# Kernel optimization log

Measured on AMD Instinct MI355X. Metric: run time of the kernel, lower is better.

The kernel has to match this reference:

```python
import math
import jax, jax.numpy as jnp
import numpy as np

D_MODEL = 256
N_HEADS = 8
D_K = D_MODEL // N_HEADS
BS = 2
SEQ = 2048
NEG = -1e32


def _linear(x, W, b):
    return x @ W + b


def _layernorm(x, g, b):
    m = jnp.mean(x, axis=-1, keepdims=True)
    v = jnp.mean((x - m) ** 2, axis=-1, keepdims=True)
    return (x - m) / jnp.sqrt(v + 1e-5) * g + b


def _attention(q, k, v, mask, gammas):
    # q,k,v: [b,h,s,dk]; mask: [1,1,s,s] bool; gammas: [h,1,1]
    d_k = q.shape[-1]
    scores = jnp.einsum('bhqd,bhkd->bhqk', q, k) / math.sqrt(d_k)
    S = scores.shape[-1]
    # distance-decay bias (computed under stop_gradient, as torch.no_grad + detach)
    sm = jax.lax.stop_gradient(jax.nn.softmax(jnp.where(mask, scores, NEG), axis=-1))
    distcum = jnp.cumsum(sm, axis=-1)
    disttot = jnp.sum(sm, axis=-1, keepdims=True)
    idx = jnp.arange(S, dtype=scores.dtype)
    pos = jnp.abs(idx[None, :] - idx[:, None])[None, None]  # |i-j|
    dist = jax.lax.stop_gradient(
        jnp.sqrt(jnp.clip((disttot - distcum) * pos, 0.0, None)))
    gamma = -jax.nn.softplus(gammas)[None]  # [1,h,1,1]
    eff = jnp.clip(jnp.exp(dist * gamma), 1e-5, 1e5)
    scores = jnp.where(mask, scores * eff, NEG)
    scores = jnp.where(mask, jax.nn.softmax(scores, axis=-1), 0.0)
    return jnp.einsum('bhqk,bhkd->bhqd', scores, v)


def _mha(qx, kx, vx, Wq, bq, Wk, bk, Wv, bv, Wo, bo, gammas, mask):
    bs = qx.shape[0]
    def split(x, W, b):
        return _linear(x, W, b).reshape(bs, -1, N_HEADS, D_K).transpose(0, 2, 1, 3)
    q = split(qx, Wq, bq)
    k = split(kx, Wk, bk)
    v = split(vx, Wv, bv)
    o = _attention(q, k, v, mask, gammas)
    o = o.transpose(0, 2, 1, 3).reshape(bs, -1, D_MODEL)
    return _linear(o, Wo, bo)


def _layer(query, key, values, Wq, bq, Wk, bk, Wv, bv, Wo, bo, gammas, ln_g, ln_b, peek_cur):
    S = query.shape[1]
    mask = jnp.tril(jnp.ones((S, S), dtype=bool), 0 if peek_cur else -1)[None, None]
    out = _mha(query, key, values, Wq, bq, Wk, bk, Wv, bv, Wo, bo, gammas, mask)
    return _layernorm(query + out, ln_g, ln_b)


def _forward(q_emb, qa_emb,
             b1_Wq, b1_bq, b1_Wv, b1_bv, b1_Wo, b1_bo, b1_gam, b1_lng, b1_lnb,
             b2_Wq, b2_bq, b2_Wv, b2_bv, b2_Wo, b2_bo, b2_gam, b2_lng, b2_lnb,
             b3_Wq, b3_bq, b3_Wk, b3_bk, b3_Wv, b3_bv, b3_Wo, b3_bo, b3_gam, b3_lng, b3_lnb,
             know_params, lk_W, lk_b, lv_W, lv_b):
    # blocks 1 & 2: kq_same -> k projection shares q projection weights
    hq = _layer(q_emb, q_emb, q_emb,
                b1_Wq, b1_bq, b1_Wq, b1_bq, b1_Wv, b1_bv, b1_Wo, b1_bo,
                b1_gam, b1_lng, b1_lnb, peek_cur=True)
    ha = _layer(qa_emb, qa_emb, qa_emb,
                b2_Wq, b2_bq, b2_Wq, b2_bq, b2_Wv, b2_bv, b2_Wo, b2_bo,
                b2_gam, b2_lng, b2_lnb, peek_cur=True)
    query = jnp.broadcast_to(know_params, hq.shape)
    h = _layer(query, hq, ha,
               b3_Wq, b3_bq, b3_Wk, b3_bk, b3_Wv, b3_bv, b3_Wo, b3_bo,
               b3_gam, b3_lng, b3_lnb, peek_cur=False)
    bs, S, d = hq.shape
    key = jax.nn.sigmoid(_linear(
        jnp.broadcast_to(know_params, (bs, S, d)).reshape(bs, S, N_HEADS, D_K),
        lk_W, lk_b)).reshape(bs * S, N_HEADS, d)
    value = jax.nn.sigmoid(_linear(
        h.reshape(bs, S, N_HEADS, D_K), lv_W, lv_b)).reshape(bs * S, N_HEADS, d)
    beta = jnp.einsum('nhd,nd->nh', key, q_emb.reshape(bs * S, d))
    alpha = jax.nn.softmax(beta, axis=-1)
    h = jnp.einsum('nh,nhd->nd', alpha, value).reshape(bs, S, d)
    return h


def setup_inputs() -> dict:
    keys = iter(jax.random.split(jax.random.key(0), 64))
    def nrm(shape, scale=0.02):
        return jax.random.normal(next(keys), shape, dtype=jnp.float32) * scale
    def uni(shape):
        return jax.random.uniform(next(keys), shape, dtype=jnp.float32, minval=-1.0, maxval=1.0)
    d = D_MODEL
    inp = {
        'q_emb': nrm((BS, SEQ, d), 1.0),
        'qa_emb': nrm((BS, SEQ, d), 1.0),
    }
    for blk in ('b1', 'b2'):
        inp[blk + '_Wq'] = nrm((d, d)); inp[blk + '_bq'] = jnp.zeros((d,), jnp.float32)
        inp[blk + '_Wv'] = nrm((d, d)); inp[blk + '_bv'] = jnp.zeros((d,), jnp.float32)
        inp[blk + '_Wo'] = nrm((d, d)); inp[blk + '_bo'] = jnp.zeros((d,), jnp.float32)
        inp[blk + '_gam'] = uni((N_HEADS, 1, 1))
        inp[blk + '_lng'] = jnp.ones((d,), jnp.float32)
        inp[blk + '_lnb'] = jnp.zeros((d,), jnp.float32)
    inp['b3_Wq'] = nrm((d, d)); inp['b3_bq'] = jnp.zeros((d,), jnp.float32)
    inp['b3_Wk'] = nrm((d, d)); inp['b3_bk'] = jnp.zeros((d,), jnp.float32)
    inp['b3_Wv'] = nrm((d, d)); inp['b3_bv'] = jnp.zeros((d,), jnp.float32)
    inp['b3_Wo'] = nrm((d, d)); inp['b3_bo'] = jnp.zeros((d,), jnp.float32)
    inp['b3_gam'] = uni((N_HEADS, 1, 1))
    inp['b3_lng'] = jnp.ones((d,), jnp.float32)
    inp['b3_lnb'] = jnp.zeros((d,), jnp.float32)
    inp['know_params'] = uni((1, 1, d))
    inp['lk_W'] = nrm((D_K, d)); inp['lk_b'] = jnp.zeros((d,), jnp.float32)
    inp['lv_W'] = nrm((D_K, d)); inp['lv_b'] = jnp.zeros((d,), jnp.float32)
    return inp


def reference(q_emb, qa_emb,
              b1_Wq, b1_bq, b1_Wv, b1_bv, b1_Wo, b1_bo, b1_gam, b1_lng, b1_lnb,
              b2_Wq, b2_bq, b2_Wv, b2_bv, b2_Wo, b2_bo, b2_gam, b2_lng, b2_lnb,
              b3_Wq, b3_bq, b3_Wk, b3_bk, b3_Wv, b3_bv, b3_Wo, b3_bo, b3_gam, b3_lng, b3_lnb,
              know_params, lk_W, lk_b, lv_W, lv_b):
    return _forward(q_emb, qa_emb,
                    b1_Wq, b1_bq, b1_Wv, b1_bv, b1_Wo, b1_bo, b1_gam, b1_lng, b1_lnb,
                    b2_Wq, b2_bq, b2_Wv, b2_bv, b2_Wo, b2_bo, b2_gam, b2_lng, b2_lnb,
                    b3_Wq, b3_bq, b3_Wk, b3_bk, b3_Wv, b3_bv, b3_Wo, b3_bo, b3_gam, b3_lng, b3_lnb,
                    know_params, lk_W, lk_b, lv_W, lv_b)
```

## Files before the change

kernel.cpp:

```cpp
#include <hip/hip_runtime.h>
#include <hip/hip_bf16.h>

#define DM 256
#define NH 8
#define DK 32
#define BSZ 2
#define SEQ 2048
#define ROWS (BSZ*SEQ)
#define RT 16
#define SRB 2312

static __device__ __forceinline__ int sw8(int j) { return j + ((j >> 6) << 3); }

typedef __attribute__((ext_vector_type(8))) short short8;
typedef __attribute__((ext_vector_type(4))) float f32x4;

static __device__ __forceinline__ unsigned short f2bf(float f) {
    unsigned u = __float_as_uint(f);
    return (unsigned short)((u + 0x7FFFu + ((u >> 16) & 1u)) >> 16);
}
static __device__ __forceinline__ float bf2f(unsigned short h) {
    return __uint_as_float(((unsigned)h) << 16);
}

static __device__ __forceinline__ unsigned cvtpk(float lo, float hi) {
    unsigned r;
    asm("v_cvt_pk_bf16_f32 %0, %1, %2" : "=v"(r) : "v"(lo), "v"(hi));
    return r;
}

static __device__ __forceinline__ float ex2(float x) { return __builtin_amdgcn_exp2f(x); }
static __device__ __forceinline__ float sqt(float x) { return __builtin_amdgcn_sqrtf(x); }
static __device__ __forceinline__ float rcp(float x) { return __builtin_amdgcn_rcpf(x); }

template<int CTRL, int RM>
static __device__ __forceinline__ float dppadd(float x) {
    int s = __builtin_amdgcn_update_dpp(0, __float_as_int(x), CTRL, RM, 0xf, true);
    return x + __int_as_float(s);
}
static __device__ __forceinline__ float scan32(float x) {
    x = dppadd<0x111, 0xf>(x);
    x = dppadd<0x112, 0xf>(x);
    x = dppadd<0x114, 0xf>(x);
    x = dppadd<0x118, 0xf>(x);
    x = dppadd<0x142, 0xa>(x);
    return x;
}
static __device__ __forceinline__ float red16(float x) {
    x = dppadd<0x0B1, 0xf>(x);
    x = dppadd<0x04E, 0xf>(x);
    x = dppadd<0x124, 0xf>(x);
    x = dppadd<0x128, 0xf>(x);
    return x;
}
static __device__ __forceinline__ float bcast31(float x) {
    return __int_as_float(__builtin_amdgcn_ds_swizzle(__float_as_int(x), 0x03E0));
}
static __device__ __forceinline__ float swz_x16(float x) {
    return __int_as_float(__builtin_amdgcn_ds_swizzle(__float_as_int(x), 0x401F));
}

static __device__ __forceinline__ void unpack4(uint2 u, float& s0, float& s1,
                                               float& s2, float& s3) {
    s0 = __uint_as_float(u.x << 16);
    s1 = __uint_as_float(u.x & 0xFFFF0000u);
    s2 = __uint_as_float(u.y << 16);
    s3 = __uint_as_float(u.y & 0xFFFF0000u);
}

static __device__ __forceinline__ uint2 decay_quad(
    float s0, float s1, float s2, float s3v,
    float e0, float e1, float e2, float e3,
    float cum, float pq, float linv,
    float l, float gamma2, float& l2)
{
    float p0, p1, p2, p3;
    cum += e0;
    { float dist = sqt(fmaxf((l - cum) * pq, 0.f));
      float eff = fmaxf(ex2(dist * gamma2), 1e-5f);
      p0 = ex2(s0 * eff); l2 += p0; }
    cum += e1;
    { float dist = sqt(fmaxf((l - cum) * (pq - linv), 0.f));
      float eff = fmaxf(ex2(dist * gamma2), 1e-5f);
      p1 = ex2(s1 * eff); l2 += p1; }
    cum += e2;
    { float dist = sqt(fmaxf((l - cum) * (pq - 2.f * linv), 0.f));
      float eff = fmaxf(ex2(dist * gamma2), 1e-5f);
      p2 = ex2(s2 * eff); l2 += p2; }
    cum += e3;
    { float dist = sqt(fmaxf((l - cum) * (pq - 3.f * linv), 0.f));
      float eff = fmaxf(ex2(dist * gamma2), 1e-5f);
      p3 = ex2(s3v * eff); l2 += p3; }
    uint2 st;
    st.x = cvtpk(p0, p1);
    st.y = cvtpk(p2, p3);
    return st;
}

#define MFMA_BF16 __builtin_amdgcn_mfma_f32_16x16x32_bf16
#define LOG2E 1.44269504088896340736f

static __device__ __forceinline__ float waveRedSum(float v) {
    #pragma unroll
    for (int off = 32; off > 0; off >>= 1) v += __shfl_down(v, off, 64);
    return v;
}

__global__ __launch_bounds__(256) void convert_w_kernel(
    const float* __restrict__ S0, const float* __restrict__ S1, const float* __restrict__ S2,
    const float* __restrict__ S3, const float* __restrict__ S4, const float* __restrict__ S5,
    const float* __restrict__ S6, const float* __restrict__ S7, const float* __restrict__ S8,
    unsigned short* __restrict__ dst)
{
    const float* W;
    int s = blockIdx.y;
    if (s == 0) W = S0; else if (s == 1) W = S1; else if (s == 2) W = S2;
    else if (s == 3) W = S3; else if (s == 4) W = S4; else if (s == 5) W = S5;
    else if (s == 6) W = S6; else if (s == 7) W = S7; else W = S8;
    unsigned short* H = dst + (size_t)s * 131072;
    unsigned short* L = H + 65536;

    int e = blockIdx.x * 1024 + threadIdx.x * 4;
    int k = e >> 8, n = e & 255;
    float4 w4 = *(const float4*)(W + e);
    float v[4] = {w4.x, w4.y, w4.z, w4.w};
    #pragma unroll
    for (int i = 0; i < 4; ++i) {
        unsigned short h = f2bf(v[i]);
        H[(size_t)(n + i) * 256 + k] = h;
        L[(size_t)(n + i) * 256 + k] = (unsigned short)f2bf(v[i] - bf2f(h));
    }
}

__global__ __launch_bounds__(256) void gemm4_kernel(
    const float* __restrict__ X0, const unsigned short* __restrict__ H0, const float* __restrict__ B0,
    float* __restrict__ Y0, unsigned short* __restrict__ K0o, unsigned short* __restrict__ V0o,
    const float* __restrict__ X1, const unsigned short* __restrict__ H1, const float* __restrict__ B1,
    float* __restrict__ Y1, unsigned short* __restrict__ K1o, unsigned short* __restrict__ V1o,
    const float* __restrict__ X2, const unsigned short* __restrict__ H2, const float* __restrict__ B2,
    float* __restrict__ Y2, unsigned short* __restrict__ K2o, unsigned short* __restrict__ V2o,
    const float* __restrict__ X3, const unsigned short* __restrict__ H3, const float* __restrict__ B3,
    float* __restrict__ Y3, unsigned short* __restrict__ K3o, unsigned short* __restrict__ V3o)
{
    const float *X, *Bias; const unsigned short* H; float* Yf;
    unsigned short *KSo, *VSo;
    int s = blockIdx.y;
    if (s == 0)      { X = X0; H = H0; Bias = B0; Yf = Y0; KSo = K0o; VSo = V0o; }
    else if (s == 1) { X = X1; H = H1; Bias = B1; Yf = Y1; KSo = K1o; VSo = V1o; }
    else if (s == 2) { X = X2; H = H2; Bias = B2; Yf = Y2; KSo = K2o; VSo = V2o; }
    else             { X = X3; H = H3; Bias = B3; Yf = Y3; KSo = K3o; VSo = V3o; }
    const unsigned short* L = H + 65536;

    __shared__ __align__(16) unsigned short XhL[16 * 264];
    __shared__ __align__(16) unsigned short XlL[16 * 264];
    int t = threadIdx.x;
    int r0 = blockIdx.x * 16;
    {
        int r = t >> 4, c0 = (t & 15) * 16;
        const float* xp = X + (size_t)(r0 + r) * DM + c0;
        #pragma unroll
        for (int i = 0; i < 16; i += 4) {
            float4 v4 = *(const float4*)(xp + i);
            float vv[4] = {v4.x, v4.y, v4.z, v4.w};
            #pragma unroll
            for (int j = 0; j < 4; ++j) {
                unsigned short h = f2bf(vv[j]);
                XhL[r * 264 + c0 + i + j] = h;
                XlL[r * 264 + c0 + i + j] = (unsigned short)f2bf(vv[j] - bf2f(h));
            }
        }
    }
    __syncthreads();
    int lane = t & 63, wv = t >> 6;
    int m = lane & 15, quad = lane >> 4;
    f32x4 aa[4];
    #pragma unroll
    for (int nt = 0; nt < 4; ++nt) { aa[nt][0]=0.f; aa[nt][1]=0.f; aa[nt][2]=0.f; aa[nt][3]=0.f; }
    #pragma unroll 1
    for (int kc = 0; kc < 8; ++kc) {
        int k0 = kc * 32;
        short8 Ah = *(const short8*)&XhL[m * 264 + k0 + quad * 8];
        short8 Al = *(const short8*)&XlL[m * 264 + k0 + quad * 8];
        size_t boff = (size_t)(wv * 64 + m) * 256 + k0 + quad * 8;
        #pragma unroll
        for (int nt = 0; nt < 4; ++nt) {
            short8 Bh = *(const short8*)(H + boff + nt * 16 * 256);
            short8 Bl = *(const short8*)(L + boff + nt * 16 * 256);
            aa[nt] = MFMA_BF16(Al, Bh, aa[nt], 0, 0, 0);
            aa[nt] = MFMA_BF16(Ah, Bl, aa[nt], 0, 0, 0);
            aa[nt] = MFMA_BF16(Ah, Bh, aa[nt], 0, 0, 0);
        }
    }
    int col0 = wv * 64 + m;
    #pragma unroll
    for (int nt = 0; nt < 4; ++nt) {
        int col = col0 + nt * 16;
        float bb = Bias[col];
        float yv[4];
        #pragma unroll
        for (int g = 0; g < 4; ++g) yv[g] = aa[nt][g] + bb;
        if (Yf) {
            #pragma unroll
            for (int g = 0; g < 4; ++g)
                Yf[(size_t)(r0 + quad * 4 + g) * DM + col] = yv[g];
        }
        if (KSo) {
            unsigned short* KH = KSo;
            unsigned short* KL = KSo + (size_t)ROWS * DM;
            #pragma unroll
            for (int g = 0; g < 4; ++g) {
                unsigned short hb = f2bf(yv[g]);
                KH[(size_t)(r0 + quad * 4 + g) * DM + col] = hb;
                KL[(size_t)(r0 + quad * 4 + g) * DM + col] =
                    (unsigned short)f2bf(yv[g] - bf2f(hb));
            }
        }
        if (VSo) {
            unsigned short* VH = VSo;
            ushort4 h4;
            h4.x = f2bf(yv[0]); h4.y = f2bf(yv[1]);
            h4.z = f2bf(yv[2]); h4.w = f2bf(yv[3]);
            *(ushort4*)&VH[(size_t)col * ROWS + r0 + quad * 4] = h4;
        }
    }
}

__global__ __launch_bounds__(256) void gemm_ln2_kernel(
    const float* __restrict__ X0, const unsigned short* __restrict__ H0, const float* __restrict__ B0,
    const float* __restrict__ R0, const float* __restrict__ G0, const float* __restrict__ L0,
    float* __restrict__ Y0, int bc0,
    const float* __restrict__ X1, const unsigned short* __restrict__ H1, const float* __restrict__ B1,
    const float* __restrict__ R1, const float* __restrict__ G1, const float* __restrict__ L1,
    float* __restrict__ Y1, int bc1)
{
    const float *X, *Bias, *R, *G, *Lb; const unsigned short* H; float* Y; int bc;
    if (blockIdx.y == 0) { X=X0; H=H0; Bias=B0; R=R0; G=G0; Lb=L0; Y=Y0; bc=bc0; }
    else                 { X=X1; H=H1; Bias=B1; R=R1; G=G1; Lb=L1; Y=Y1; bc=bc1; }
    const unsigned short* L = H + 65536;

    __shared__ __align__(16) unsigned short XhL[16 * 264];
    __shared__ __align__(16) unsigned short XlL[16 * 264];
    __shared__ __align__(16) float yl[16 * 260];
    int t = threadIdx.x;
    int r0 = blockIdx.x * 16;
    {   int r = t >> 4, c0 = (t & 15) * 16;
        const float* xp = X + (size_t)(r0 + r) * DM + c0;
        #pragma unroll
        for (int i = 0; i < 16; i += 4) {
            float4 v4 = *(const float4*)(xp + i);
            float vv[4] = {v4.x, v4.y, v4.z, v4.w};
            #pragma unroll
            for (int j = 0; j < 4; ++j) {
                unsigned short h = f2bf(vv[j]);
                XhL[r * 264 + c0 + i + j] = h;
                XlL[r * 264 + c0 + i + j] = (unsigned short)f2bf(vv[j] - bf2f(h));
            }
        }
    }
    __syncthreads();
    int lane = t & 63, wv = t >> 6;
    int m = lane & 15, quad = lane >> 4;
    f32x4 aa[4];
    #pragma unroll
    for (int nt = 0; nt < 4; ++nt) { aa[nt][0]=0.f; aa[nt][1]=0.f; aa[nt][2]=0.f; aa[nt][3]=0.f; }
    #pragma unroll 1
    for (int kc = 0; kc < 8; ++kc) {
        int k0 = kc * 32;
        short8 Ah = *(const short8*)&XhL[m * 264 + k0 + quad * 8];
        short8 Al = *(const short8*)&XlL[m * 264 + k0 + quad * 8];
        size_t boff = (size_t)(wv * 64 + m) * 256 + k0 + quad * 8;
        #pragma unroll
        for (int nt = 0; nt < 4; ++nt) {
            short8 Bh = *(const short8*)(H + boff + nt * 16 * 256);
            short8 Bl = *(const short8*)(L + boff + nt * 16 * 256);
            aa[nt] = MFMA_BF16(Al, Bh, aa[nt], 0, 0, 0);
            aa[nt] = MFMA_BF16(Ah, Bl, aa[nt], 0, 0, 0);
            aa[nt] = MFMA_BF16(Ah, Bh, aa[nt], 0, 0, 0);
        }
    }
    {
        int col0 = wv * 64 + m;
        #pragma unroll
        for (int nt = 0; nt < 4; ++nt) {
            int col = col0 + nt * 16;
            float bb = Bias[col];
            #pragma unroll
            for (int g = 0; g < 4; ++g) {
                int row = quad * 4 + g;
                float res = bc ? R[col] : R[(size_t)(r0 + row) * DM + col];
                yl[row * 260 + col] = aa[nt][g] + bb + res;
            }
        }
    }
    __syncthreads();
    {
        int r = t >> 4, c0 = (t & 15) * 16;
        float vals[16];
        float part = 0.f;
        #pragma unroll
        for (int i = 0; i < 16; ++i) { vals[i] = yl[r * 260 + c0 + i]; part += vals[i]; }
        #pragma unroll
        for (int off = 8; off; off >>= 1) part += __shfl_xor(part, off, 16);
        float mean = part * (1.f / DM);
        float vp = 0.f;
        #pragma unroll
        for (int i = 0; i < 16; ++i) { float d = vals[i] - mean; vp += d * d; }
        #pragma unroll
        for (int off = 8; off; off >>= 1) vp += __shfl_xor(vp, off, 16);
        float rs = rsqrtf(vp * (1.f / DM) + 1e-5f);
        float* yp = Y + (size_t)(r0 + r) * DM + c0;
        #pragma unroll
        for (int i = 0; i < 16; i += 4) {
            float4 o;
            o.x = (vals[i+0] - mean) * rs * G[c0+i+0] + Lb[c0+i+0];
            o.y = (vals[i+1] - mean) * rs * G[c0+i+1] + Lb[c0+i+1];
            o.z = (vals[i+2] - mean) * rs * G[c0+i+2] + Lb[c0+i+2];
            o.w = (vals[i+3] - mean) * rs * G[c0+i+3] + Lb[c0+i+3];
            *(float4*)(yp + i) = o;
        }
    }
}

__global__ __launch_bounds__(256) void score3_kernel(
    const float* __restrict__ q3row, const float* __restrict__ K3,
    unsigned short* __restrict__ S3, float* __restrict__ C3)
{
    __shared__ float wsum[4];
    int bh = blockIdx.x;
    int b = bh >> 3, h = bh & 7;
    int t = threadIdx.x;
    int lane = t & 63, wv = t >> 6;
    const float scaleL2 = 0.17677669529663687f * LOG2E;
    float q[DK];
    #pragma unroll
    for (int d = 0; d < DK; ++d) q[d] = q3row[h * DK + d] * scaleL2;
    size_t kb = ((size_t)b * SEQ) * DM + h * DK;
    float einc[8];
    unsigned short sb[8];
    float run = 0.f;
    #pragma unroll 1
    for (int k = 0; k < 8; ++k) {
        int j = t * 8 + k;
        const float* kp = K3 + kb + (size_t)j * DM;
        float s = 0.f;
        #pragma unroll
        for (int d = 0; d < DK; ++d) s += q[d] * kp[d];
        unsigned short sb16 = f2bf(s);
        sb[k] = sb16;
        run += ex2(bf2f(sb16));
        einc[k] = run;
    }
    float x = run;
    #pragma unroll
    for (int off = 1; off < 64; off <<= 1) {
        float y = __shfl_up(x, off, 64);
        if (lane >= off) x += y;
    }
    if (lane == 63) wsum[wv] = x;
    __syncthreads();
    float woff = 0.f;
    for (int w = 0; w < wv; ++w) woff += wsum[w];
    float pre = woff + x - run;
    #pragma unroll
    for (int k = 0; k < 8; ++k) {
        int j = t * 8 + k;
        S3[(size_t)bh * SEQ + j] = sb[k];
        C3[(size_t)bh * SEQ + j] = pre + einc[k];
    }
}

__global__ __launch_bounds__(512) void attn_tile_kernel(
    const float* __restrict__ Q0,
    const unsigned short* __restrict__ KS0, const unsigned short* __restrict__ VS0,
    const float* __restrict__ g0, float* __restrict__ O0,
    const float* __restrict__ Q1,
    const unsigned short* __restrict__ KS1, const unsigned short* __restrict__ VS1,
    const float* __restrict__ g1, float* __restrict__ O1,
    const unsigned short* __restrict__ S3g, const float* __restrict__ C3g,
    int peek, int qbcast)
{
    __shared__ __align__(16) unsigned short SB[RT * SRB];
    __shared__ float qs[RT][DK];
    __shared__ float l2inv_s[RT];
    __shared__ float rowsum[8 * RT];

    int y = blockIdx.y;
    int set = y >> 4, bh = y & 15;
    const float* Q = set ? Q1 : Q0;
    const unsigned short* KS = set ? KS1 : KS0;
    const unsigned short* VS = set ? VS1 : VS0;
    const float* gm = set ? g1 : g0;
    float* O = set ? O1 : O0;

    int b = bh >> 3, h = bh & 7;
    int i0 = ((int)gridDim.x - 1 - (int)blockIdx.x) * RT;
    int t = threadIdx.x;
    size_t base = ((size_t)b * SEQ) * DM + (size_t)h * DK;

    int njAll = peek ? (i0 + RT) : (i0 + RT - 1);
    int njPad32 = (njAll + 31) & ~31;
    int njPad128 = (njAll + 127) & ~127;
    const float scaleL2 = 0.17677669529663687f * LOG2E;

    if (!qbcast) {
        {
            int r = t >> 5, d = t & 31;
            qs[r][d] = Q[base + (size_t)(i0 + r) * DM + d];
        }
        __syncthreads();

        {
            int wave = t >> 6, lane = t & 63;
            int m = lane & 15, quad = lane >> 4;

            float av[8];
            {
                float4 qa = *(const float4*)&qs[m][8 * quad];
                float4 qb = *(const float4*)&qs[m][8 * quad + 4];
                av[0]=qa.x*scaleL2; av[1]=qa.y*scaleL2; av[2]=qa.z*scaleL2; av[3]=qa.w*scaleL2;
                av[4]=qb.x*scaleL2; av[5]=qb.y*scaleL2; av[6]=qb.z*scaleL2; av[7]=qb.w*scaleL2;
            }
            short8 Ah;
            #pragma unroll
            for (int i = 0; i < 8; ++i) Ah[i] = (short)f2bf(av[i]);

            const unsigned short* KH = KS;
            const unsigned short* KL = KS + (size_t)ROWS * DM;
            size_t rowb = (size_t)b * SEQ;
            int njr0 = i0 + quad * 4 + peek;
            float rp0 = 0.f, rp1 = 0.f, rp2 = 0.f, rp3 = 0.f;
            int nChunks = (njAll + 15) >> 4;
            #pragma unroll 1
            for (int c = wave; c < nChunks; c += 8) {
                int j0 = c << 4;
                size_t off = (rowb + j0 + m) * DM + h * DK + quad * 8;
                short8 Bh = *(const short8*)&KH[off];
                short8 Bl = *(const short8*)&KL[off];
                f32x4 acc = {0.f, 0.f, 0.f, 0.f};
                acc = MFMA_BF16(Ah, Bl, acc, 0, 0, 0);
                acc = MFMA_BF16(Ah, Bh, acc, 0, 0, 0);
                int jcol = j0 + m;
                int sj = sw8(jcol);
                unsigned pk01 = cvtpk(acc[0], acc[1]);
                unsigned pk23 = cvtpk(acc[2], acc[3]);
                SB[(quad * 4 + 0) * SRB + sj] = (unsigned short)pk01;
                SB[(quad * 4 + 1) * SRB + sj] = (unsigned short)(pk01 >> 16);
                SB[(quad * 4 + 2) * SRB + sj] = (unsigned short)pk23;
                SB[(quad * 4 + 3) * SRB + sj] = (unsigned short)(pk23 >> 16);
                rp0 += (jcol < njr0 + 0) ? ex2(acc[0]) : 0.f;
                rp1 += (jcol < njr0 + 1) ? ex2(acc[1]) : 0.f;
                rp2 += (jcol < njr0 + 2) ? ex2(acc[2]) : 0.f;
                rp3 += (jcol < njr0 + 3) ? ex2(acc[3]) : 0.f;
            }
            rp0 = red16(rp0); rp1 = red16(rp1);
            rp2 = red16(rp2); rp3 = red16(rp3);
            if (m == 0) {
                rowsum[wave * RT + quad * 4 + 0] = rp0;
                rowsum[wave * RT + quad * 4 + 1] = rp1;
                rowsum[wave * RT + quad * 4 + 2] = rp2;
                rowsum[wave * RT + quad * 4 + 3] = rp3;
            }
        }
        __syncthreads();

        {
            int r = t >> 5, c = t & 31;
            int i = i0 + r;
            int nj = peek ? (i + 1) : i;
            for (int j = nj + c; j < njPad128; j += 32)
                SB[r * SRB + sw8(j)] = 0xFF80u;
        }
        __syncthreads();
    }

    if (qbcast) {
        int r = t >> 5, c = t & 31;
        int i = i0 + r;
        int nj = peek ? (i + 1) : i;
        unsigned short* Sr = SB + r * SRB;
        float gamma2 = -log1pf(__expf(gm[h])) * LOG2E;
        const unsigned short* s3p = S3g + (size_t)bh * SEQ;
        const float* c3p = C3g + (size_t)bh * SEQ;
        float Lc = (nj > 0) ? c3p[nj - 1] : 0.f;
        float linv = (nj > 0) ? rcp(Lc) : 0.f;
        float li2 = linv + linv, li3 = li2 + linv;
        float l2 = 0.f;
        #pragma unroll 1
        for (int k = 0; 128 * k < njPad32; ++k) {
            int j4 = 128 * k + 4 * c;
            uint2 su = *(const uint2*)&s3p[j4];
            float4 C4 = *(const float4*)&c3p[j4];
            float s0 = __uint_as_float(su.x << 16);
            float s1 = __uint_as_float(su.x & 0xFFFF0000u);
            float s2 = __uint_as_float(su.y << 16);
            float s3v = __uint_as_float(su.y & 0xFFFF0000u);
            float pq = (float)(i - j4) * linv;
            float p0, p1, p2, p3;
            { float dist = sqt(fmaxf((Lc - C4.x) * pq, 0.f));
              float eff = fmaxf(ex2(dist * gamma2), 1e-5f);
              p0 = (j4 + 0 < nj) ? ex2(s0 * eff) : 0.f; l2 += p0; }
            { float dist = sqt(fmaxf((Lc - C4.y) * (pq - linv), 0.f));
              float eff = fmaxf(ex2(dist * gamma2), 1e-5f);
              p1 = (j4 + 1 < nj) ? ex2(s1 * eff) : 0.f; l2 += p1; }
            { float dist = sqt(fmaxf((Lc - C4.z) * (pq - li2), 0.f));
              float eff = fmaxf(ex2(dist * gamma2), 1e-5f);
              p2 = (j4 + 2 < nj) ? ex2(s2 * eff) : 0.f; l2 += p2; }
            { float dist = sqt(fmaxf((Lc - C4.w) * (pq - li3), 0.f));
              float eff = fmaxf(ex2(dist * gamma2), 1e-5f);
              p3 = (j4 + 3 < nj) ? ex2(s3v * eff) : 0.f; l2 += p3; }
            uint2 st;
            st.x = cvtpk(p0, p1);
            st.y = cvtpk(p2, p3);
            *(uint2*)&Sr[sw8(j4)] = st;
        }
        l2 = red16(l2);
        l2 += swz_x16(l2);
        if (c == 0) l2inv_s[r] = (nj > 0) ? rcp(l2) : 0.f;
    } else {
        int r = t >> 5, c = t & 31;
        int i = i0 + r;
        int nj = peek ? (i + 1) : i;
        unsigned short* Sr = SB + r * SRB;
        float gamma2 = -log1pf(__expf(gm[h])) * LOG2E;

        float l = 0.f;
        #pragma unroll
        for (int w = 0; w < 8; ++w) l += rowsum[w * RT + r];
        float linv = rcp(l);

        float l2 = 0.f;
        float Bc = 0.f;
        int nIter = (njPad32 + 127) >> 7;
        int pairs = nIter >> 1;
        #pragma unroll 1
        for (int k = 0; k < pairs; ++k) {
            int j4a = 256 * k + 4 * c;
            int j4b = j4a + 128;
            uint2 uA = *(const uint2*)&Sr[sw8(j4a)];
            uint2 uB = *(const uint2*)&Sr[sw8(j4b)];
            float a0, a1, a2, a3, b0, b1, b2, b3;
            unpack4(uA, a0, a1, a2, a3);
            unpack4(uB, b0, b1, b2, b3);
            float eA0 = ex2(a0), eA1 = ex2(a1), eA2 = ex2(a2), eA3 = ex2(a3);
            float eB0 = ex2(b0), eB1 = ex2(b1), eB2 = ex2(b2), eB3 = ex2(b3);
            float sigA = eA0 + eA1 + eA2 + eA3;
            float sigB = eB0 + eB1 + eB2 + eB3;
            float xA = scan32(sigA);
            float xB = scan32(sigB);
            float totA = bcast31(xA);
            float totB = bcast31(xB);
            float cumA = Bc + (xA - sigA);
            float cumB = Bc + totA + (xB - sigB);
            Bc += totA + totB;
            float pqA = (float)(i - j4a) * linv;
            float pqB = pqA - 128.f * linv;
            uint2 stA = decay_quad(a0, a1, a2, a3, eA0, eA1, eA2, eA3,
                                   cumA, pqA, linv, l, gamma2, l2);
            uint2 stB = decay_quad(b0, b1, b2, b3, eB0, eB1, eB2, eB3,
                                   cumB, pqB, linv, l, gamma2, l2);
            *(uint2*)&Sr[sw8(j4a)] = stA;
            *(uint2*)&Sr[sw8(j4b)] = stB;
        }
        if (nIter & 1) {
            int j4a = 256 * pairs + 4 * c;
            uint2 uA = *(const uint2*)&Sr[sw8(j4a)];
            float a0, a1, a2, a3;
            unpack4(uA, a0, a1, a2, a3);
            float eA0 = ex2(a0), eA1 = ex2(a1), eA2 = ex2(a2), eA3 = ex2(a3);
            float sigA = eA0 + eA1 + eA2 + eA3;
            float xA = scan32(sigA);
            float cumA = Bc + (xA - sigA);
            float pqA = (float)(i - j4a) * linv;
            uint2 stA = decay_quad(a0, a1, a2, a3, eA0, eA1, eA2, eA3,
                                   cumA, pqA, linv, l, gamma2, l2);
            *(uint2*)&Sr[sw8(j4a)] = stA;
        }
        l2 = red16(l2);
        l2 += swz_x16(l2);
        if (c == 0) l2inv_s[r] = (nj > 0) ? rcp(l2) : 0.f;
    }
    __syncthreads();

    {
        int wave = t >> 6, lane = t & 63;
        int n16 = lane & 15, quad = lane >> 4;
        const unsigned short* VH = VS;
        size_t vb0 = (size_t)(h * DK + n16) * ROWS + (size_t)b * SEQ;
        size_t vb1 = (size_t)(h * DK + 16 + n16) * ROWS + (size_t)b * SEQ;
        f32x4 oc0 = {0.f,0.f,0.f,0.f}, oc1 = {0.f,0.f,0.f,0.f};
        #pragma unroll 1
        for (int j0 = wave * 32; j0 < njPad32; j0 += 256) {
            short8 Ap = *(const short8*)&SB[n16 * SRB + sw8(j0 + quad * 8)];
            int jo = j0 + quad * 8;
            short8 Bh0 = *(const short8*)&VH[vb0 + jo];
            short8 Bh1 = *(const short8*)&VH[vb1 + jo];
            oc0 = MFMA_BF16(Ap, Bh0, oc0, 0, 0, 0);
            oc1 = MFMA_BF16(Ap, Bh1, oc1, 0, 0, 0);
        }
        __syncthreads();
        float* FS = (float*)SB;
        {
            #pragma unroll
            for (int g = 0; g < 4; ++g) {
                int row = quad * 4 + g;
                FS[wave * 512 + row * 32 + n16] = oc0[g];
                FS[wave * 512 + row * 32 + 16 + n16] = oc1[g];
            }
        }
    }
    __syncthreads();
    {
        float* FS = (float*)SB;
        int r2 = t >> 5, d = t & 31;
        float sum = 0.f;
        #pragma unroll
        for (int w = 0; w < 8; ++w)
            sum += FS[w * 512 + r2 * 32 + d];
        int ii = i0 + r2;
        O[base + (size_t)ii * DM + d] = sum * l2inv_s[r2];
    }
}

__global__ __launch_bounds__(256) void precompute_kernel(
    const float* __restrict__ know,
    const float* __restrict__ W3q, const float* __restrict__ b3q,
    const float* __restrict__ lkW, const float* __restrict__ lkb,
    float* __restrict__ q3row, float* __restrict__ key8)
{
    __shared__ float kn[DM];
    int t = threadIdx.x;
    kn[t] = know[t];
    __syncthreads();
    float acc = b3q[t];
    for (int c = 0; c < DM; ++c) acc += kn[c] * W3q[(size_t)c * DM + t];
    q3row[t] = acc;
    float bk = lkb[t];
    for (int h = 0; h < NH; ++h) {
        float a = bk;
        #pragma unroll
        for (int c = 0; c < DK; ++c) a += kn[h * DK + c] * lkW[(size_t)c * DM + t];
        key8[(size_t)h * DM + t] = 1.f / (1.f + __expf(-a));
    }
}

__global__ __launch_bounds__(256) void readout_kernel(
    const float* __restrict__ h3, const float* __restrict__ qe,
    const float* __restrict__ key8,
    const float* __restrict__ lvW, const float* __restrict__ lvb,
    float* __restrict__ out)
{
    __shared__ float hrow[DM], qrow[DM];
    __shared__ float red8[4][NH];
    int n = blockIdx.x, t = threadIdx.x;
    int lane = t & 63, wid = t >> 6;
    hrow[t] = h3[(size_t)n * DM + t];
    qrow[t] = qe[(size_t)n * DM + t];
    __syncthreads();
    float ph[NH];
    #pragma unroll
    for (int h = 0; h < NH; ++h) {
        float v = key8[(size_t)h * DM + t] * qrow[t];
        v = waveRedSum(v);
        ph[h] = v;
    }
    if (lane == 0) {
        #pragma unroll
        for (int h = 0; h < NH; ++h) red8[wid][h] = ph[h];
    }
    __syncthreads();
    float beta[NH];
    #pragma unroll
    for (int h = 0; h < NH; ++h)
        beta[h] = red8[0][h] + red8[1][h] + red8[2][h] + red8[3][h];
    float bv = lvb[t];
    float vh[NH];
    for (int h = 0; h < NH; ++h) {
        float a = bv;
        #pragma unroll
        for (int c = 0; c < DK; ++c) a += hrow[h * DK + c] * lvW[(size_t)c * DM + t];
        vh[h] = 1.f / (1.f + __expf(-a));
    }
    float mb = beta[0];
    #pragma unroll
    for (int h = 1; h < NH; ++h) mb = fmaxf(mb, beta[h]);
    float se = 0.f, eh[NH];
    #pragma unroll
    for (int h = 0; h < NH; ++h) { eh[h] = __expf(beta[h] - mb); se += eh[h]; }
    float sinv = 1.f / se;
    float o = 0.f;
    #pragma unroll
    for (int h = 0; h < NH; ++h) o += eh[h] * sinv * vh[h];
    out[(size_t)n * DM + t] = o;
}

extern "C" void kernel_launch(void* const* d_in, const int* in_sizes, int n_in,
                              void* d_out, int out_size, void* d_ws, size_t ws_size,
                              hipStream_t stream) {
    (void)in_sizes; (void)n_in; (void)out_size; (void)ws_size;
    const float* q_emb  = (const float*)d_in[0];
    const float* qa_emb = (const float*)d_in[1];
    const float* b1_Wq = (const float*)d_in[2];
    const float* b1_bq = (const float*)d_in[3];
    const float* b1_Wv = (const float*)d_in[4];
    const float* b1_bv = (const float*)d_in[5];
    const float* b1_Wo = (const float*)d_in[6];
    const float* b1_bo = (const float*)d_in[7];
    const float* b1_gam = (const float*)d_in[8];
    const float* b1_lng = (const float*)d_in[9];
    const float* b1_lnb = (const float*)d_in[10];
    const float* b2_Wq = (const float*)d_in[11];
    const float* b2_bq = (const float*)d_in[12];
    const float* b2_Wv = (const float*)d_in[13];
    const float* b2_bv = (const float*)d_in[14];
    const float* b2_Wo = (const float*)d_in[15];
    const float* b2_bo = (const float*)d_in[16];
    const float* b2_gam = (const float*)d_in[17];
    const float* b2_lng = (const float*)d_in[18];
    const float* b2_lnb = (const float*)d_in[19];
    const float* b3_Wq = (const float*)d_in[20];
    const float* b3_bq = (const float*)d_in[21];
    const float* b3_Wk = (const float*)d_in[22];
    const float* b3_bk = (const float*)d_in[23];
    const float* b3_Wv = (const float*)d_in[24];
    const float* b3_bv = (const float*)d_in[25];
    const float* b3_Wo = (const float*)d_in[26];
    const float* b3_bo = (const float*)d_in[27];
    const float* b3_gam = (const float*)d_in[28];
    const float* b3_lng = (const float*)d_in[29];
    const float* b3_lnb = (const float*)d_in[30];
    const float* know  = (const float*)d_in[31];
    const float* lk_W  = (const float*)d_in[32];
    const float* lk_b  = (const float*)d_in[33];
    const float* lv_W  = (const float*)d_in[34];
    const float* lv_b  = (const float*)d_in[35];

    const size_t SLAB = (size_t)ROWS * DM;
    const size_t USLAB = 2 * SLAB;
    float* A1 = (float*)d_ws;
    float* A2 = A1 + SLAB;
    float* C1 = A2 + SLAB;
    float* C2 = C1 + SLAB;
    unsigned short* KS1 = (unsigned short*)(C2 + SLAB);
    unsigned short* KS2 = KS1 + USLAB;
    unsigned short* VS1 = KS2 + USLAB;
    unsigned short* VS2 = VS1 + USLAB;
    float* q3row = (float*)(VS2 + USLAB);
    float* key8  = q3row + DM;
    unsigned short* Wsp = (unsigned short*)(key8 + NH * DM);
    unsigned short* S3buf = Wsp + (size_t)9 * 131072;
    float* C3buf = (float*)(S3buf + 16 * SEQ);
    float* hq = (float*)KS1;
    float* ha = (float*)KS2;
    float* k3 = A1;
    unsigned short* VS3 = VS1;
    float* O3 = C1;
    float* h3 = C2;

    auto WH = [&](int i) { return Wsp + (size_t)i * 131072; };

    dim3 blk(256);
    dim3 ablk(512);
    dim3 agrid2(SEQ / RT, 32);
    dim3 agrid1(SEQ / RT, 16);
    dim3 rgrid(ROWS);

    convert_w_kernel<<<dim3(64, 9), blk, 0, stream>>>(
        b1_Wq, b1_Wv, b1_Wo, b2_Wq, b2_Wv, b2_Wo, b3_Wk, b3_Wv, b3_Wo, Wsp);

    precompute_kernel<<<dim3(1), blk, 0, stream>>>(know, b3_Wq, b3_bq, lk_W, lk_b, q3row, key8);

    gemm4_kernel<<<dim3(ROWS/16, 4), blk, 0, stream>>>(
        q_emb,  WH(0), b1_bq, A1,      KS1,     nullptr,
        q_emb,  WH(1), b1_bv, nullptr, nullptr, VS1,
        qa_emb, WH(3), b2_bq, A2,      KS2,     nullptr,
        qa_emb, WH(4), b2_bv, nullptr, nullptr, VS2);

    attn_tile_kernel<<<agrid2, ablk, 0, stream>>>(
        A1, KS1, VS1, b1_gam, C1,
        A2, KS2, VS2, b2_gam, C2,
        nullptr, nullptr, 1, 0);

    gemm_ln2_kernel<<<dim3(ROWS/16, 2), blk, 0, stream>>>(
        C1, WH(2), b1_bo, q_emb,  b1_lng, b1_lnb, hq, 0,
        C2, WH(5), b2_bo, qa_emb, b2_lng, b2_lnb, ha, 0);

    gemm4_kernel<<<dim3(ROWS/16, 2), blk, 0, stream>>>(
        hq, WH(6), b3_bk, k3,      nullptr, nullptr,
        ha, WH(7), b3_bv, nullptr, nullptr, VS3,
        hq, WH(6), b3_bk, k3,      nullptr, nullptr,
        hq, WH(6), b3_bk, k3,      nullptr, nullptr);

    score3_kernel<<<dim3(16), blk, 0, stream>>>(q3row, k3, S3buf, C3buf);

    attn_tile_kernel<<<agrid1, ablk, 0, stream>>>(
        q3row, nullptr, VS3, b3_gam, O3,
        q3row, nullptr, VS3, b3_gam, O3,
        S3buf, C3buf, 0, 1);

    gemm_ln2_kernel<<<dim3(ROWS/16, 1), blk, 0, stream>>>(
        O3, WH(8), b3_bo, know, b3_lng, b3_lnb, h3, 1,
        O3, WH(8), b3_bo, know, b3_lng, b3_lnb, h3, 1);

    readout_kernel<<<rgrid, blk, 0, stream>>>(h3, q_emb, key8, lv_W, lv_b,
                                              (float*)d_out);
}
```

Measured before the change: 467.5 us.

## Split block-3 score/prefix-sum kernel across sequence blocks and unroll attention loops

Replaces the 16-block score3 kernel, where each thread serially handled 8 keys, with a two-pass scheme. The first pass uses 128 blocks, one key per thread, and writes per-block totals. The second pass adds the carried-in offsets. This exposes more parallelism for a small serial stage but adds a kernel launch and an extra read-modify-write of C3. It also sets unroll 2 on three inner attention loops to allow more loads in flight, at some register-pressure risk.

```diff
diff --git a/kernel.cpp b/kernel.cpp
--- a/kernel.cpp
+++ b/kernel.cpp
@@ -321,36 +321,39 @@
     }
 }
 
-__global__ __launch_bounds__(256) void score3_kernel(
+__global__ __launch_bounds__(256) void score3a_kernel(
     const float* __restrict__ q3row, const float* __restrict__ K3,
-    unsigned short* __restrict__ S3, float* __restrict__ C3)
+    unsigned short* __restrict__ S3, float* __restrict__ C3,
+    float* __restrict__ Csum)
 {
     __shared__ float wsum[4];
-    int bh = blockIdx.x;
+    int s = blockIdx.x;
+    int bh = blockIdx.y;
     int b = bh >> 3, h = bh & 7;
     int t = threadIdx.x;
     int lane = t & 63, wv = t >> 6;
+    int j = s * 256 + t;
     const float scaleL2 = 0.17677669529663687f * LOG2E;
-    float q[DK];
-    #pragma unroll
-    for (int d = 0; d < DK; ++d) q[d] = q3row[h * DK + d] * scaleL2;
-    size_t kb = ((size_t)b * SEQ) * DM + h * DK;
-    float einc[8];
-    unsigned short sb[8];
-    float run = 0.f;
-    #pragma unroll 1
-    for (int k = 0; k < 8; ++k) {
-        int j = t * 8 + k;
-        const float* kp = K3 + kb + (size_t)j * DM;
-        float s = 0.f;
-        #pragma unroll
-        for (int d = 0; d < DK; ++d) s += q[d] * kp[d];
-        unsigned short sb16 = f2bf(s);
-        sb[k] = sb16;
-        run += ex2(bf2f(sb16));
-        einc[k] = run;
-    }
-    float x = run;
+    float qv[DK];
+    #pragma unroll
+    for (int d = 0; d < DK; d += 4) {
+        float4 qq = *(const float4*)(q3row + h * DK + d);
+        qv[d+0] = qq.x * scaleL2; qv[d+1] = qq.y * scaleL2;
+        qv[d+2] = qq.z * scaleL2; qv[d+3] = qq.w * scaleL2;
+    }
+    const float* kp = K3 + ((size_t)b * SEQ + j) * DM + h * DK;
+    float kv[DK];
+    #pragma unroll
+    for (int d = 0; d < DK; d += 4) {
+        float4 kq = *(const float4*)(kp + d);
+        kv[d+0] = kq.x; kv[d+1] = kq.y; kv[d+2] = kq.z; kv[d+3] = kq.w;
+    }
+    float sc = 0.f;
+    #pragma unroll
+    for (int d = 0; d < DK; ++d) sc += qv[d] * kv[d];
+    unsigned short sb16 = f2bf(sc);
+    float e = ex2(bf2f(sb16));
+    float x = e;
     #pragma unroll
     for (int off = 1; off < 64; off <<= 1) {
         float y = __shfl_up(x, off, 64);
@@ -360,13 +363,21 @@
     __syncthreads();
     float woff = 0.f;
     for (int w = 0; w < wv; ++w) woff += wsum[w];
-    float pre = woff + x - run;
-    #pragma unroll
-    for (int k = 0; k < 8; ++k) {
-        int j = t * 8 + k;
-        S3[(size_t)bh * SEQ + j] = sb[k];
-        C3[(size_t)bh * SEQ + j] = pre + einc[k];
-    }
+    float inc = woff + x;
+    S3[(size_t)bh * SEQ + j] = sb16;
+    C3[(size_t)bh * SEQ + j] = inc;
+    if (t == 255) Csum[bh * 8 + s] = inc;
+}
+
+__global__ __launch_bounds__(256) void score3b_kernel(
+    const float* __restrict__ Csum, float* __restrict__ C3)
+{
+    int s = blockIdx.x + 1;
+    int bh = blockIdx.y;
+    int t = threadIdx.x;
+    float off = 0.f;
+    for (int w = 0; w < s; ++w) off += Csum[bh * 8 + w];
+    C3[(size_t)bh * SEQ + s * 256 + t] += off;
 }
 
 __global__ __launch_bounds__(512) void attn_tile_kernel(
@@ -430,7 +441,7 @@
             int njr0 = i0 + quad * 4 + peek;
             float rp0 = 0.f, rp1 = 0.f, rp2 = 0.f, rp3 = 0.f;
             int nChunks = (njAll + 15) >> 4;
-            #pragma unroll 1
+            #pragma unroll 2
             for (int c = wave; c < nChunks; c += 8) {
                 int j0 = c << 4;
                 size_t off = (rowb + j0 + m) * DM + h * DK + quad * 8;
@@ -485,7 +496,7 @@
         float linv = (nj > 0) ? rcp(Lc) : 0.f;
         float li2 = linv + linv, li3 = li2 + linv;
         float l2 = 0.f;
-        #pragma unroll 1
+        #pragma unroll 2
         for (int k = 0; 128 * k < njPad32; ++k) {
             int j4 = 128 * k + 4 * c;
             uint2 su = *(const uint2*)&s3p[j4];
@@ -588,7 +599,7 @@
         size_t vb0 = (size_t)(h * DK + n16) * ROWS + (size_t)b * SEQ;
         size_t vb1 = (size_t)(h * DK + 16 + n16) * ROWS + (size_t)b * SEQ;
         f32x4 oc0 = {0.f,0.f,0.f,0.f}, oc1 = {0.f,0.f,0.f,0.f};
-        #pragma unroll 1
+        #pragma unroll 2
         for (int j0 = wave * 32; j0 < njPad32; j0 += 256) {
             short8 Ap = *(const short8*)&SB[n16 * SRB + sw8(j0 + quad * 8)];
             int jo = j0 + quad * 8;
@@ -749,6 +760,7 @@
     unsigned short* Wsp = (unsigned short*)(key8 + NH * DM);
     unsigned short* S3buf = Wsp + (size_t)9 * 131072;
     float* C3buf = (float*)(S3buf + 16 * SEQ);
+    float* Csum  = C3buf + 16 * SEQ;
     float* hq = (float*)KS1;
     float* ha = (float*)KS2;
     float* k3 = A1;
@@ -790,7 +802,8 @@
         hq, WH(6), b3_bk, k3,      nullptr, nullptr,
         hq, WH(6), b3_bk, k3,      nullptr, nullptr);
 
-    score3_kernel<<<dim3(16), blk, 0, stream>>>(q3row, k3, S3buf, C3buf);
+    score3a_kernel<<<dim3(8, 16), blk, 0, stream>>>(q3row, k3, S3buf, C3buf, Csum);
+    score3b_kernel<<<dim3(7, 16), blk, 0, stream>>>(Csum, C3buf);
 
     attn_tile_kernel<<<agrid1, ablk, 0, stream>>>(
         q3row, nullptr, VS3, b3_gam, O3,
```

New measurement: 458.2 us. 1.02x faster.
